# Kernel optimization log

Hardware: AMD Instinct MI355X
Metric: run time of the kernel (lower is better)

The kernel has to match this reference:

```python
import jax, jax.numpy as jnp
import numpy as np

EPS = 1e-5
K = 20
MAXV = 64


def knn_idx(x, k):
    # x: [B,N,D] -> idx: [B,N,k] (excluding self, matching torch topk of -dist)
    xx = jnp.sum(x * x, axis=-1, keepdims=True)                      # [B,N,1]
    dist = xx - 2.0 * jnp.einsum('bnd,bmd->bnm', x, x) + jnp.swapaxes(xx, 1, 2)
    _, idx = jax.lax.top_k(-dist, k + 1)
    return idx[:, :, 1:]


def edge_conv(x, W, gamma, beta, mean, var, k):
    # x: [B,N,C]; W: [O,2C]; BN in eval mode; max over k neighbors
    idx = knn_idx(x, k)                                              # [B,N,k]
    nbr = jax.vmap(lambda xi, ii: xi[ii])(x, idx)                    # [B,N,k,C]
    ctr = jnp.broadcast_to(x[:, :, None, :], nbr.shape)
    ef = jnp.concatenate([ctr, nbr - ctr], axis=-1)                  # [B,N,k,2C]
    y = jnp.einsum('bnkc,oc->bnko', ef, W)                           # 1x1 conv
    y = (y - mean) * (gamma * jax.lax.rsqrt(var + EPS)) + beta       # BN eval
    y = jnp.where(y >= 0, y, 0.2 * y)                                # LeakyReLU
    return jnp.max(y, axis=2)                                        # [B,N,O]


def setup_inputs() -> dict:
    key = jax.random.key(0)
    ks = jax.random.split(key, 32)
    f32 = jnp.float32
    def w(k_, o, i):
        return jax.random.normal(k_, (o, i), f32) / np.float32(np.sqrt(i))
    def vec(k_, c):
        return jax.random.normal(k_, (c,), f32) * 0.1
    d = {}
    d['x'] = jax.random.normal(ks[0], (4, 8192, 5), f32)
    # EdgeConv 1: 5 -> 32
    d['W1'] = w(ks[1], 32, 10)
    d['g1'] = jax.random.uniform(ks[2], (32,), f32, 0.5, 1.5)
    d['b1'] = vec(ks[3], 32); d['m1'] = vec(ks[4], 32)
    d['v1'] = jax.random.uniform(ks[5], (32,), f32, 0.5, 1.5)
    # EdgeConv 2: 32 -> 64
    d['W2'] = w(ks[6], 64, 64)
    d['g2'] = jax.random.uniform(ks[7], (64,), f32, 0.5, 1.5)
    d['b2'] = vec(ks[8], 64); d['m2'] = vec(ks[9], 64)
    d['v2'] = jax.random.uniform(ks[10], (64,), f32, 0.5, 1.5)
    # EdgeConv 3: 64 -> 128
    d['W3'] = w(ks[11], 128, 128)
    d['g3'] = jax.random.uniform(ks[12], (128,), f32, 0.5, 1.5)
    d['b3'] = vec(ks[13], 128); d['m3'] = vec(ks[14], 128)
    d['v3'] = jax.random.uniform(ks[15], (128,), f32, 0.5, 1.5)
    # conv_global: 224 -> 256
    d['Wg'] = w(ks[16], 256, 224)
    d['gg'] = jax.random.uniform(ks[17], (256,), f32, 0.5, 1.5)
    d['bg'] = vec(ks[18], 256); d['mg'] = vec(ks[19], 256)
    d['vg'] = jax.random.uniform(ks[20], (256,), f32, 0.5, 1.5)
    # vertex predictor heads
    d['Wv1'] = w(ks[21], 512, 256); d['bv1'] = vec(ks[22], 512)
    d['Wv2'] = w(ks[23], 192, 512); d['bv2'] = vec(ks[24], 192)
    d['Wq1'] = w(ks[25], 64, 256); d['bq1'] = vec(ks[26], 64)
    d['Wq2'] = w(ks[27], 1, 64); d['bq2'] = vec(ks[28], 1)
    return d


def reference(x, W1, g1, b1, m1, v1, W2, g2, b2, m2, v2, W3, g3, b3, m3, v3,
              Wg, gg, bg, mg, vg, Wv1, bv1, Wv2, bv2, Wq1, bq1, Wq2, bq2):
    B = x.shape[0]
    x1 = edge_conv(x, W1, g1, b1, m1, v1, K)      # [B,N,32]
    x2 = edge_conv(x1, W2, g2, b2, m2, v2, K)     # [B,N,64]
    x3 = edge_conv(x2, W3, g3, b3, m3, v3, K)     # [B,N,128]
    x_concat = jnp.concatenate([x1, x2, x3], axis=2)               # [B,N,224]
    xg = jnp.einsum('bnc,oc->bno', x_concat, Wg)                   # 1x1 conv1d
    xg = (xg - mg) * (gg * jax.lax.rsqrt(vg + EPS)) + bg
    xg = jnp.where(xg >= 0, xg, 0.2 * xg)
    gfeat = jnp.max(xg, axis=1)                                    # [B,256]
    h = jax.nn.relu(gfeat @ Wv1.T + bv1)                           # Dropout=eval id
    vertex_coords = (h @ Wv2.T + bv2).reshape(B, MAXV, 3)
    q = jax.nn.relu(gfeat @ Wq1.T + bq1)
    nvs = jax.nn.sigmoid(q @ Wq2.T + bq2)                          # [B,1]
    num_vertices = jnp.clip(jnp.round(nvs * MAXV), 1, MAXV).astype(jnp.int32)
    return (vertex_coords, num_vertices[:, 0], nvs[:, 0], gfeat, x_concat)
```

## Files before the change

kernel.cpp:

```cpp
#include <hip/hip_runtime.h>
#include <hip/hip_bf16.h>


#define NPTS 8192
#define BATCH 4
#define KNBR 20

typedef _Float16 half8 __attribute__((ext_vector_type(8)));
typedef float f32x4 __attribute__((ext_vector_type(4)));

__device__ __forceinline__ int cswz(int r, int nc) {
    return (nc == 8) ? (r & 7) : ((r >> 1) & 3);
}
__device__ __forceinline__ int dswz(int q) { return (q >> 1) & 7; }

template <int D, int DK, int RS, int S>
__global__ __launch_bounds__(128, 2) void knn_part_mfma(
    const float* feat, float* xcat) {
    constexpr int TJ  = 32;
    constexpr int BUF = 12;
    constexpr int JC  = NPTS / S;
    constexpr int NC  = DK / 8;
    constexpr int KS  = DK / 32;
    constexpr int DSTR = 32;
    constexpr int RSF = (D % 4 == 0) ? D : 9;
    constexpr int REGA = 16384;
    constexpr int OFF_XJF = REGA;
    constexpr int OFF_XJH = OFF_XJF + ((TJ * RSF * 4 + 15) & ~15);
    constexpr int OFF_XXJ = OFF_XJH + TJ * DK * 2;
    constexpr int OFF_SXJ = OFF_XXJ + JC * 4;
    constexpr int OFF_BUF = OFF_SXJ + JC * 4;
    constexpr int OFF_MEA = OFF_BUF + BUF * 128 * 2;
    constexpr int OFF_TMX = OFF_MEA + ((D * 4 + 15) & ~15);
    __shared__ __align__(16) char smem[OFF_TMX + (JC / TJ) * 4];

    float*          dist = (float*)smem;
    _Float16*       xih  = (_Float16*)smem;
    float*          xjf  = (float*)(smem + OFF_XJF);
    _Float16*       xjh  = (_Float16*)(smem + OFF_XJH);
    float*          xxj  = (float*)(smem + OFF_XXJ);
    float*          sxj  = (float*)(smem + OFF_SXJ);
    unsigned short* bufj = (unsigned short*)(smem + OFF_BUF);
    float*          meanp= (float*)(smem + OFF_MEA);
    float*          tmax = (float*)(smem + OFF_TMX);

    const int tid   = threadIdx.x;
    const int gi    = blockIdx.x * 128 + tid;
    const int s     = blockIdx.y;
    const int b     = gi >> 13;
    const int ib    = gi & (NPTS - 1);
    const int n0b   = (blockIdx.x * 128) & (NPTS - 1);
    const int sbase = s * JC;
    const float* fb = feat + (size_t)b * NPTS * RS;

    const float C1 = 0.001953125f;
    const float C2 = 1.52587890625e-05f;

    float xi[D];
    if (D % 4 == 0) {
        #pragma unroll
        for (int c4 = 0; c4 < D / 4; ++c4) {
            float4 v = *(const float4*)(fb + (size_t)ib * RS + 4 * c4);
            xi[4 * c4] = v.x; xi[4 * c4 + 1] = v.y;
            xi[4 * c4 + 2] = v.z; xi[4 * c4 + 3] = v.w;
        }
    } else {
        #pragma unroll
        for (int c = 0; c < D; ++c) xi[c] = fb[(size_t)ib * RS + c];
    }
    float xxi = 0.f;
    #pragma unroll
    for (int c = 0; c < D; ++c) xxi = fmaf(xi[c], xi[c], xxi);

    if (tid < D) meanp[tid] = fb[(size_t)n0b * RS + tid];
    __syncthreads();

    float s_i = 0.f;
    #pragma unroll
    for (int c = 0; c < D; ++c) {
        float d = xi[c] - meanp[c];
        s_i = fmaf(d, d, s_i);
    }
    const float off_i = fmaf(C1, s_i, C2 * xxi) - s_i;

    for (int e = tid; e < 128 * NC; e += 128) {
        int r = e / NC, c = e % NC;
        const float* row = fb + (size_t)(n0b + r) * RS;
        half8 h;
        if (D % 8 == 0) {
            float4 v0 = *(const float4*)(row + c * 8);
            float4 v1 = *(const float4*)(row + c * 8 + 4);
            float4 m0 = *(const float4*)(meanp + c * 8);
            float4 m1 = *(const float4*)(meanp + c * 8 + 4);
            h[0] = (_Float16)(v0.x - m0.x); h[1] = (_Float16)(v0.y - m0.y);
            h[2] = (_Float16)(v0.z - m0.z); h[3] = (_Float16)(v0.w - m0.w);
            h[4] = (_Float16)(v1.x - m1.x); h[5] = (_Float16)(v1.y - m1.y);
            h[6] = (_Float16)(v1.z - m1.z); h[7] = (_Float16)(v1.w - m1.w);
        } else {
            #pragma unroll
            for (int t = 0; t < 8; ++t) {
                int dim = c * 8 + t;
                h[t] = (dim < D) ? (_Float16)(row[dim] - meanp[dim])
                                 : (_Float16)0.f;
            }
        }
        *(half8*)(xih + (size_t)r * DK + (c ^ cswz(r, NC)) * 8) = h;
    }

    for (int r = tid; r < JC; r += 128) {
        const float* row = fb + (size_t)(sbase + r) * RS;
        float sm = 0.f, sc = 0.f;
        if (D % 4 == 0) {
            #pragma unroll
            for (int c4 = 0; c4 < D / 4; ++c4) {
                float4 v = *(const float4*)(row + 4 * c4);
                sm = fmaf(v.x, v.x, sm); sm = fmaf(v.y, v.y, sm);
                sm = fmaf(v.z, v.z, sm); sm = fmaf(v.w, v.w, sm);
                float4 m = *(const float4*)(meanp + 4 * c4);
                float d0 = v.x - m.x, d1 = v.y - m.y;
                float d2 = v.z - m.z, d3 = v.w - m.w;
                sc = fmaf(d0, d0, sc); sc = fmaf(d1, d1, sc);
                sc = fmaf(d2, d2, sc); sc = fmaf(d3, d3, sc);
            }
        } else {
            #pragma unroll
            for (int c = 0; c < D; ++c) {
                float v = row[c];
                sm = fmaf(v, v, sm);
                float d = v - meanp[c];
                sc = fmaf(d, d, sc);
            }
        }
        xxj[r] = sm;
        sxj[r] = sc;
    }
    __syncthreads();

    const int lane = tid & 63, wid = tid >> 6;
    const int ln = lane & 15, lg = lane >> 4;
    half8 bfr[4][KS];
    #pragma unroll
    for (int qs = 0; qs < 4; ++qs)
        #pragma unroll
        for (int ks = 0; ks < KS; ++ks) {
            int q = wid * 64 + qs * 16 + ln;
            bfr[qs][ks] = *(const half8*)(
                xih + (size_t)q * DK + (((lg + 4 * ks) ^ cswz(q, NC)) * 8));
        }

    if (tid < JC / TJ) {
        float mx = -__builtin_inff();
        for (int r = 0; r < TJ; ++r) {
            int j = tid * TJ + ((r + tid) & (TJ - 1));
            mx = fmaxf(mx, fmaf(C1, sxj[j], C2 * xxj[j]));
        }
        tmax[tid] = mx;
    }

    float dl[21];
    int   il[21];
    #pragma unroll
    for (int t = 0; t < 21; ++t) { dl[t] = __builtin_inff(); il[t] = 0; }
    float thr_t  = __builtin_inff();
    float tmaxcur = 0.f;
    int   cnt = 0;
    int   j0s = 0;

    auto insert1 = [&](int u) {
        if (u < cnt) {
            int jsp = (int)bufj[u * 128 + tid];
            int jl  = jsp - j0s;
            const float* row = xjf + (size_t)jl * RSF;
            float dot = 0.f;
            if (D % 4 == 0) {
                int fsw = jl & 7;
                #pragma unroll
                for (int c4 = 0; c4 < D / 4; ++c4) {
                    float4 v = *(const float4*)(row + ((c4 ^ fsw) * 4));
                    dot = fmaf(xi[4 * c4 + 0], v.x, dot);
                    dot = fmaf(xi[4 * c4 + 1], v.y, dot);
                    dot = fmaf(xi[4 * c4 + 2], v.z, dot);
                    dot = fmaf(xi[4 * c4 + 3], v.w, dot);
                }
            } else {
                #pragma unroll
                for (int c = 0; c < D; ++c) dot = fmaf(xi[c], row[c], dot);
            }
            float dd = __builtin_fmaf(-2.f, dot, xxi + xxj[jsp]);
            if (dd < dl[20]) {
                dl[20] = dd; il[20] = sbase + jsp;
                #pragma unroll
                for (int t = 20; t > 0; --t) {
                    if (dl[t] < dl[t - 1]) {
                        float td = dl[t]; dl[t] = dl[t - 1]; dl[t - 1] = td;
                        int   ti = il[t]; il[t] = il[t - 1]; il[t - 1] = ti;
                    }
                }
            }
        }
    };
    auto drain = [&]() {
        #pragma unroll 1
        for (int u = 0; __any(u < cnt); u += 2) {
            insert1(u);
            insert1(u + 1);
        }
        cnt = 0;
        thr_t = dl[20] + off_i + tmaxcur;
    };

    #pragma unroll 1
    for (int t0 = 0; t0 < JC; t0 += TJ) {
        j0s = t0;
        __syncthreads();
        if (D % 8 == 0) {
            for (int e = tid; e < TJ * NC; e += 128) {
                int r = e / NC, c = e % NC;
                const float* row = fb + (size_t)(sbase + t0 + r) * RS + c * 8;
                float4 v0 = *(const float4*)(row);
                float4 v1 = *(const float4*)(row + 4);
                int fsw = r & 7;
                *(float4*)(xjf + (size_t)r * RSF + (((2 * c)     ^ fsw) * 4)) = v0;
                *(float4*)(xjf + (size_t)r * RSF + (((2 * c + 1) ^ fsw) * 4)) = v1;
                float4 m0 = *(const float4*)(meanp + c * 8);
                float4 m1 = *(const float4*)(meanp + c * 8 + 4);
                half8 h;
                h[0] = (_Float16)(v0.x - m0.x); h[1] = (_Float16)(v0.y - m0.y);
                h[2] = (_Float16)(v0.z - m0.z); h[3] = (_Float16)(v0.w - m0.w);
                h[4] = (_Float16)(v1.x - m1.x); h[5] = (_Float16)(v1.y - m1.y);
                h[6] = (_Float16)(v1.z - m1.z); h[7] = (_Float16)(v1.w - m1.w);
                *(half8*)(xjh + (size_t)r * DK + ((c ^ cswz(r, NC)) * 8)) = h;
            }
        } else {
            for (int e = tid; e < TJ * NC; e += 128) {
                int r = e / NC, c = e % NC;
                const float* row = fb + (size_t)(sbase + t0 + r) * RS;
                half8 h;
                #pragma unroll
                for (int q2 = 0; q2 < 8; ++q2) {
                    int dim = c * 8 + q2;
                    float f = (dim < D) ? row[dim] : 0.f;
                    h[q2] = (dim < D) ? (_Float16)(f - meanp[dim])
                                      : (_Float16)0.f;
                    if (c == 0 && q2 < D) xjf[(size_t)r * RSF + q2] = f;
                }
                *(half8*)(xjh + (size_t)r * DK + ((c ^ cswz(r, NC)) * 8)) = h;
            }
        }
        __syncthreads();
        tmaxcur = tmax[t0 >> 5];
        thr_t   = dl[20] + off_i + tmaxcur;

        #pragma unroll
        for (int js = 0; js < TJ / 16; ++js) {
            half8 afr[KS];
            #pragma unroll
            for (int ks = 0; ks < KS; ++ks) {
                int jr = js * 16 + ln;
                afr[ks] = *(const half8*)(
                    xjh + (size_t)jr * DK +
                    (((lg + 4 * ks) ^ cswz(jr, NC)) * 8));
            }
            #pragma unroll
            for (int qs = 0; qs < 4; ++qs) {
                f32x4 acc = {0.f, 0.f, 0.f, 0.f};
                #pragma unroll
                for (int ks = 0; ks < KS; ++ks)
                    acc = __builtin_amdgcn_mfma_f32_16x16x32_f16(
                        afr[ks], bfr[qs][ks], acc, 0, 0, 0);
                float4 sv;
                sv.x = -2.f * acc[0];
                sv.y = -2.f * acc[1];
                sv.z = -2.f * acc[2];
                sv.w = -2.f * acc[3];
                int q  = wid * 64 + qs * 16 + ln;
                int ck = js * 4 + lg;
                *(float4*)(dist + (size_t)q * DSTR + ((ck ^ dswz(q)) * 4)) = sv;
            }
        }
        __syncthreads();

        {
            float* drow = dist + (size_t)tid * DSTR;
            int dsw = dswz(tid);
            #pragma unroll 1
            for (int c = 0; c < TJ / 4; ++c) {
                if (__any(cnt > BUF - 4)) drain();
                float4 sx4 = *(const float4*)(sxj + t0 + c * 4);
                float4 sv  = *(const float4*)(drow + ((c ^ dsw) * 4));
                int jb = t0 + c * 4;
                if (sv.x + sx4.x < thr_t) { bufj[cnt * 128 + tid] = (unsigned short)(jb);     ++cnt; }
                if (sv.y + sx4.y < thr_t) { bufj[cnt * 128 + tid] = (unsigned short)(jb + 1); ++cnt; }
                if (sv.z + sx4.z < thr_t) { bufj[cnt * 128 + tid] = (unsigned short)(jb + 2); ++cnt; }
                if (sv.w + sx4.w < thr_t) { bufj[cnt * 128 + tid] = (unsigned short)(jb + 3); ++cnt; }
            }
            drain();
        }
    }

    unsigned short* cp =
        (unsigned short*)(xcat + (size_t)gi * 224 + 96) + s * 21;
    #pragma unroll
    for (int t = 0; t < 21; ++t) cp[t] = (unsigned short)il[t];
}

template <int D, int RS, int S>
__global__ __launch_bounds__(256) void knn_merge(
    const float* feat, const float* xcat, unsigned short* __restrict__ idxout) {
    int gi = blockIdx.x * 256 + threadIdx.x;
    int b  = gi >> 13;
    int ib = gi & (NPTS - 1);
    const float* fb = feat + (size_t)b * NPTS * RS;

    float xi[D];
    if (D % 4 == 0) {
        #pragma unroll
        for (int c4 = 0; c4 < D / 4; ++c4) {
            float4 v = *(const float4*)(fb + (size_t)ib * RS + 4 * c4);
            xi[4 * c4] = v.x; xi[4 * c4 + 1] = v.y;
            xi[4 * c4 + 2] = v.z; xi[4 * c4 + 3] = v.w;
        }
    } else {
        #pragma unroll
        for (int c = 0; c < D; ++c) xi[c] = fb[(size_t)ib * RS + c];
    }
    float xxi = 0.f;
    #pragma unroll
    for (int c = 0; c < D; ++c) xxi = fmaf(xi[c], xi[c], xxi);

    const unsigned short* cp =
        (const unsigned short*)(xcat + (size_t)gi * 224 + 96);

    float dl[21];
    int   il[21];
    #pragma unroll
    for (int t = 0; t < 21; ++t) { dl[t] = __builtin_inff(); il[t] = 0; }

    for (int t = 0; t < S * 21; ++t) {
        int j = ((int)cp[t]) & (NPTS - 1);
        const float* row = fb + (size_t)j * RS;
        float dot = 0.f, xx = 0.f;
        if (D % 4 == 0) {
            #pragma unroll
            for (int c4 = 0; c4 < D / 4; ++c4) {
                float4 v = *(const float4*)(row + 4 * c4);
                dot = fmaf(xi[4 * c4], v.x, dot);     xx = fmaf(v.x, v.x, xx);
                dot = fmaf(xi[4 * c4 + 1], v.y, dot); xx = fmaf(v.y, v.y, xx);
                dot = fmaf(xi[4 * c4 + 2], v.z, dot); xx = fmaf(v.z, v.z, xx);
                dot = fmaf(xi[4 * c4 + 3], v.w, dot); xx = fmaf(v.w, v.w, xx);
            }
        } else {
            #pragma unroll
            for (int c = 0; c < D; ++c) {
                float v = row[c];
                dot = fmaf(xi[c], v, dot);
                xx  = fmaf(v, v, xx);
            }
        }
        float d = __builtin_fmaf(-2.f, dot, xxi + xx);
        if (d < dl[20]) {
            dl[20] = d; il[20] = j;
            #pragma unroll
            for (int u = 20; u > 0; --u) {
                if (dl[u] < dl[u - 1]) {
                    float td = dl[u]; dl[u] = dl[u - 1]; dl[u - 1] = td;
                    int   ti = il[u]; il[u] = il[u - 1]; il[u - 1] = ti;
                }
            }
        }
    }
    unsigned short* op = idxout + (size_t)gi * KNBR;
    #pragma unroll
    for (int t = 1; t < 21; ++t) op[t - 1] = (unsigned short)il[t];
}

template <int CIN, int RS, int COUT, int OTILE, int P>
__global__ __launch_bounds__(256) void edgeconv_kernel(
    const float* feat, const unsigned short* __restrict__ knn,
    const float* __restrict__ W, const float* __restrict__ g,
    const float* __restrict__ beta, const float* __restrict__ mu,
    const float* __restrict__ var,
    float* outb, int concat_off) {
    __shared__ float diff[P][KNBR][CIN];
    __shared__ float xil[P][CIN];
    __shared__ unsigned short kidx[P * KNBR];
    __shared__ float sl[OTILE], bl[OTILE], ml[OTILE];

    int tid = threadIdx.x;
    int h   = blockIdx.y;
    int n0  = blockIdx.x * P;
    int b   = n0 >> 13;
    const float* fbase = feat + ((size_t)b << 13) * RS;

    for (int e = tid; e < P * CIN; e += 256)
        xil[e / CIN][e % CIN] = feat[(size_t)(n0 + e / CIN) * RS + e % CIN];
    for (int e = tid; e < P * KNBR; e += 256)
        kidx[e] = knn[(size_t)(n0 + e / KNBR) * KNBR + e % KNBR] & (NPTS - 1);
    for (int e = tid; e < OTILE; e += 256) {
        int o = h * OTILE + e;
        sl[e] = g[o] * rsqrtf(var[o] + 1e-5f);
        bl[e] = beta[o];
        ml[e] = mu[o];
    }
    __syncthreads();

    if (CIN % 4 == 0) {
        for (int e = tid; e < P * KNBR * (CIN / 4); e += 256) {
            int r = e / (CIN / 4), c4 = e % (CIN / 4);
            int p = r / KNBR, k = r % KNBR;
            int j = (int)kidx[r];
            float4 v = *(const float4*)(fbase + (size_t)j * RS + 4 * c4);
            diff[p][k][4 * c4 + 0] = v.x - xil[p][4 * c4 + 0];
            diff[p][k][4 * c4 + 1] = v.y - xil[p][4 * c4 + 1];
            diff[p][k][4 * c4 + 2] = v.z - xil[p][4 * c4 + 2];
            diff[p][k][4 * c4 + 3] = v.w - xil[p][4 * c4 + 3];
        }
    } else {
        for (int e = tid; e < P * KNBR * CIN; e += 256) {
            int r = e / CIN, c = e % CIN;
            int pp = r / KNBR, k = r % KNBR;
            int j = (int)kidx[r];
            diff[pp][k][c] = fbase[(size_t)j * RS + c] - xil[pp][c];
        }
    }
    __syncthreads();

    int ol = tid % OTILE, p = tid / OTILE;
    int o  = h * OTILE + ol;

    float wreg[CIN];
    #pragma unroll
    for (int c = 0; c < CIN; ++c) wreg[c] = W[(size_t)o * (2 * CIN) + c];
    float a = 0.f;
    #pragma unroll
    for (int c = 0; c < CIN; ++c) a = fmaf(wreg[c], xil[p][c], a);
    #pragma unroll
    for (int c = 0; c < CIN; ++c) wreg[c] = W[(size_t)o * (2 * CIN) + CIN + c];

    float s = sl[ol], mm = ml[ol], bb = bl[ol];
    float best = -__builtin_inff();
    for (int k = 0; k < KNBR; ++k) {
        float ac0 = a, ac1 = 0.f, ac2 = 0.f, ac3 = 0.f;
        #pragma unroll
        for (int c = 0; c < CIN; ++c) {
            float d = diff[p][k][c];
            if ((c & 3) == 0)      ac0 = fmaf(wreg[c], d, ac0);
            else if ((c & 3) == 1) ac1 = fmaf(wreg[c], d, ac1);
            else if ((c & 3) == 2) ac2 = fmaf(wreg[c], d, ac2);
            else                   ac3 = fmaf(wreg[c], d, ac3);
        }
        float acc = ((ac0 + ac1) + ac2) + ac3;
        float y = (acc - mm) * s + bb;
        y = (y >= 0.f) ? y : 0.2f * y;
        best = fmaxf(best, y);
    }
    outb[(size_t)(n0 + p) * 224 + concat_off + o] = best;
}

__global__ __launch_bounds__(256) void convglobal_kernel(
    const float* __restrict__ xcat,
    const float* __restrict__ Wg, const float* __restrict__ gg,
    const float* __restrict__ bg, const float* __restrict__ mg,
    const float* __restrict__ vg,
    float* __restrict__ partial) {
    const int KC = 56, PT = 64, OT = 64, ST = 68;
    __shared__ float flT[KC * ST];
    __shared__ float WlT[KC * ST];
    __shared__ float red[64 * 17];

    int tid = threadIdx.x;
    int oi  = tid & 15, pi = tid >> 4;
    int o0  = blockIdx.y * OT;
    int n0  = blockIdx.x * PT;
    int b   = n0 >> 13;
    int pchunk = blockIdx.x & 127;

    float acc[4][4];
    #pragma unroll
    for (int u = 0; u < 4; ++u)
        #pragma unroll
        for (int v = 0; v < 4; ++v) acc[u][v] = 0.f;

    for (int kc = 0; kc < 224; kc += KC) {
        __syncthreads();
        for (int e = tid; e < PT * (KC / 4); e += 256) {
            int p = e / (KC / 4), c4 = e % (KC / 4);
            float4 v = *(const float4*)(xcat + (size_t)(n0 + p) * 224 + kc + 4 * c4);
            flT[(4 * c4 + 0) * ST + p] = v.x;
            flT[(4 * c4 + 1) * ST + p] = v.y;
            flT[(4 * c4 + 2) * ST + p] = v.z;
            flT[(4 * c4 + 3) * ST + p] = v.w;
        }
        for (int e = tid; e < OT * (KC / 4); e += 256) {
            int o = e / (KC / 4), c4 = e % (KC / 4);
            float4 v = *(const float4*)(Wg + (size_t)(o0 + o) * 224 + kc + 4 * c4);
            WlT[(4 * c4 + 0) * ST + o] = v.x;
            WlT[(4 * c4 + 1) * ST + o] = v.y;
            WlT[(4 * c4 + 2) * ST + o] = v.z;
            WlT[(4 * c4 + 3) * ST + o] = v.w;
        }
        __syncthreads();
        #pragma unroll 8
        for (int c = 0; c < KC; ++c) {
            float4 w4 = *(const float4*)(WlT + c * ST + oi * 4);
            float4 f4 = *(const float4*)(flT + c * ST + pi * 4);
            acc[0][0] = fmaf(w4.x, f4.x, acc[0][0]);
            acc[0][1] = fmaf(w4.x, f4.y, acc[0][1]);
            acc[0][2] = fmaf(w4.x, f4.z, acc[0][2]);
            acc[0][3] = fmaf(w4.x, f4.w, acc[0][3]);
            acc[1][0] = fmaf(w4.y, f4.x, acc[1][0]);
            acc[1][1] = fmaf(w4.y, f4.y, acc[1][1]);
            acc[1][2] = fmaf(w4.y, f4.z, acc[1][2]);
            acc[1][3] = fmaf(w4.y, f4.w, acc[1][3]);
            acc[2][0] = fmaf(w4.z, f4.x, acc[2][0]);
            acc[2][1] = fmaf(w4.z, f4.y, acc[2][1]);
            acc[2][2] = fmaf(w4.z, f4.z, acc[2][2]);
            acc[2][3] = fmaf(w4.z, f4.w, acc[2][3]);
            acc[3][0] = fmaf(w4.w, f4.x, acc[3][0]);
            acc[3][1] = fmaf(w4.w, f4.y, acc[3][1]);
            acc[3][2] = fmaf(w4.w, f4.z, acc[3][2]);
            acc[3][3] = fmaf(w4.w, f4.w, acc[3][3]);
        }
    }
    #pragma unroll
    for (int u = 0; u < 4; ++u) {
        int oL = oi * 4 + u, o = o0 + oL;
        float s = gg[o] * rsqrtf(vg[o] + 1e-5f);
        float mm = mg[o], bb = bg[o];
        float best = -__builtin_inff();
        #pragma unroll
        for (int v = 0; v < 4; ++v) {
            float y = (acc[u][v] - mm) * s + bb;
            y = (y >= 0.f) ? y : 0.2f * y;
            best = fmaxf(best, y);
        }
        red[oL * 17 + pi] = best;
    }
    __syncthreads();
    if (tid < 64) {
        float best = -__builtin_inff();
        #pragma unroll
        for (int q = 0; q < 16; ++q) best = fmaxf(best, red[tid * 17 + q]);
        partial[((size_t)(b * 128 + pchunk)) * 256 + o0 + tid] = best;
    }
}

__global__ void reduce_gfeat_kernel(const float* __restrict__ partial,
                                    float* __restrict__ gfeat,
                                    float* __restrict__ outg) {
    int b = blockIdx.x, o = threadIdx.x;
    float best = -__builtin_inff();
    for (int ch = 0; ch < 128; ++ch)
        best = fmaxf(best, partial[((size_t)b * 128 + ch) * 256 + o]);
    gfeat[b * 256 + o] = best;
    outg[b * 256 + o]  = best;
}

__global__ __launch_bounds__(256) void heads_kernel(
    const float* __restrict__ gfeat,
    const float* __restrict__ Wv1, const float* __restrict__ bv1,
    const float* __restrict__ Wv2, const float* __restrict__ bv2,
    const float* __restrict__ Wq1, const float* __restrict__ bq1,
    const float* __restrict__ Wq2, const float* __restrict__ bq2,
    float* __restrict__ out) {
    int b = blockIdx.x, t = threadIdx.x;
    __shared__ float gf[256], h[512], q[64];
    gf[t] = gfeat[b * 256 + t];
    __syncthreads();
    for (int r = t; r < 512; r += 256) {
        float acc = bv1[r];
        for (int c = 0; c < 256; ++c) acc = fmaf(Wv1[r * 256 + c], gf[c], acc);
        h[r] = fmaxf(acc, 0.f);
    }
    __syncthreads();
    if (t < 192) {
        float acc = bv2[t];
        for (int c = 0; c < 512; ++c) acc = fmaf(Wv2[t * 512 + c], h[c], acc);
        out[b * 192 + t] = acc;
    } else {
        int r = t - 192;
        if (r < 64) {
            float acc = bq1[r];
            for (int c = 0; c < 256; ++c) acc = fmaf(Wq1[r * 256 + c], gf[c], acc);
            q[r] = fmaxf(acc, 0.f);
        }
    }
    __syncthreads();
    if (t == 0) {
        float acc = bq2[0];
        for (int c = 0; c < 64; ++c) acc = fmaf(Wq2[c], q[c], acc);
        float nv = 1.0f / (1.0f + expf(-acc));
        out[772 + b] = nv;
        float num = fminf(fmaxf(rintf(nv * 64.0f), 1.0f), 64.0f);
        out[768 + b] = num;
    }
}

extern "C" void kernel_launch(void* const* d_in, const int* in_sizes, int n_in,
                              void* d_out, int out_size, void* d_ws, size_t ws_size,
                              hipStream_t stream) {
    (void)in_sizes; (void)n_in; (void)out_size; (void)ws_size;
    const float* x   = (const float*)d_in[0];
    const float* W1  = (const float*)d_in[1];
    const float* g1  = (const float*)d_in[2];
    const float* b1  = (const float*)d_in[3];
    const float* m1  = (const float*)d_in[4];
    const float* v1  = (const float*)d_in[5];
    const float* W2  = (const float*)d_in[6];
    const float* g2  = (const float*)d_in[7];
    const float* b2  = (const float*)d_in[8];
    const float* m2  = (const float*)d_in[9];
    const float* v2  = (const float*)d_in[10];
    const float* W3  = (const float*)d_in[11];
    const float* g3  = (const float*)d_in[12];
    const float* b3  = (const float*)d_in[13];
    const float* m3  = (const float*)d_in[14];
    const float* v3  = (const float*)d_in[15];
    const float* Wg  = (const float*)d_in[16];
    const float* gg  = (const float*)d_in[17];
    const float* bg  = (const float*)d_in[18];
    const float* mg  = (const float*)d_in[19];
    const float* vg  = (const float*)d_in[20];
    const float* Wv1 = (const float*)d_in[21];
    const float* bv1 = (const float*)d_in[22];
    const float* Wv2 = (const float*)d_in[23];
    const float* bv2 = (const float*)d_in[24];
    const float* Wq1 = (const float*)d_in[25];
    const float* bq1 = (const float*)d_in[26];
    const float* Wq2 = (const float*)d_in[27];
    const float* bq2 = (const float*)d_in[28];

    float* out  = (float*)d_out;
    float* xcat = out + 1800;
    char* ws = (char*)d_ws;
    const int ROWS = BATCH * NPTS;

    unsigned short* idx  = (unsigned short*)(ws);
    float*          part = (float*)(ws);
    float*          gft  = (float*)(ws + 524288);

    knn_part_mfma<5, 32, 5, 8><<<dim3(ROWS / 128, 8), 128, 0, stream>>>(x, xcat);
    knn_merge<5, 5, 8><<<ROWS / 256, 256, 0, stream>>>(x, xcat, idx);
    edgeconv_kernel<5, 5, 32, 32, 8>
        <<<dim3(ROWS / 8, 1), 256, 0, stream>>>(x, idx, W1, g1, b1, m1, v1, xcat, 0);

    knn_part_mfma<32, 32, 224, 8><<<dim3(ROWS / 128, 8), 128, 0, stream>>>(xcat, xcat);
    knn_merge<32, 224, 8><<<ROWS / 256, 256, 0, stream>>>(xcat, xcat, idx);
    edgeconv_kernel<32, 224, 64, 64, 4>
        <<<dim3(ROWS / 4, 1), 256, 0, stream>>>(xcat, idx, W2, g2, b2, m2, v2, xcat, 32);

    knn_part_mfma<64, 64, 224, 8><<<dim3(ROWS / 128, 8), 128, 0, stream>>>(xcat + 32, xcat);
    knn_merge<64, 224, 8><<<ROWS / 256, 256, 0, stream>>>(xcat + 32, xcat, idx);
    edgeconv_kernel<64, 224, 128, 64, 4>
        <<<dim3(ROWS / 4, 2), 256, 0, stream>>>(xcat + 32, idx, W3, g3, b3, m3, v3, xcat, 96);

    convglobal_kernel<<<dim3(ROWS / 64, 4), 256, 0, stream>>>(
        xcat, Wg, gg, bg, mg, vg, part);
    reduce_gfeat_kernel<<<BATCH, 256, 0, stream>>>(part, gft, out + 776);

    heads_kernel<<<BATCH, 256, 0, stream>>>(
        gft, Wv1, bv1, Wv2, bv2, Wq1, bq1, Wq2, bq2, out);
}
```

Baseline: 4.202 ms.

## Two-pass fp16 distance threshold candidate filter for KNN partial search

The per-slice KNN kernel now keeps approximate fp16 distances (with the centred-norm term folded in) and runs two passes over the tiles. The first pass builds a top-21 bound from the approximate distances. The second recomputes the tiles and records every candidate under a conservative error-widened threshold, up to 31 per slice, with an overflow flag. The merge kernel then computes exact fp32 distances only for those candidates, or scans the whole slice when the flag is set. This removes the in-loop exact dot products and drain buffers from the partial kernel, at the cost of computing the MFMA tiles twice. Correctness depends on the fp16 error bound constant C1, which was lowered.

```diff
diff --git a/kernel.cpp b/kernel.cpp
--- a/kernel.cpp
+++ b/kernel.cpp
@@ -7,40 +7,35 @@
 #define KNBR 20
 
 typedef _Float16 half8 __attribute__((ext_vector_type(8)));
+typedef _Float16 half4 __attribute__((ext_vector_type(4)));
 typedef float f32x4 __attribute__((ext_vector_type(4)));
 
 __device__ __forceinline__ int cswz(int r, int nc) {
     return (nc == 8) ? (r & 7) : ((r >> 1) & 3);
 }
-__device__ __forceinline__ int dswz(int q) { return (q >> 1) & 7; }
 
 template <int D, int DK, int RS, int S>
 __global__ __launch_bounds__(128, 2) void knn_part_mfma(
     const float* feat, float* xcat) {
     constexpr int TJ  = 32;
-    constexpr int BUF = 12;
+    constexpr int CAP = 31;
+    constexpr int BSTR= 33;
     constexpr int JC  = NPTS / S;
+    constexpr int NT  = JC / TJ;
     constexpr int NC  = DK / 8;
     constexpr int KS  = DK / 32;
-    constexpr int DSTR = 32;
-    constexpr int RSF = (D % 4 == 0) ? D : 9;
-    constexpr int REGA = 16384;
-    constexpr int OFF_XJF = REGA;
-    constexpr int OFF_XJH = OFF_XJF + ((TJ * RSF * 4 + 15) & ~15);
-    constexpr int OFF_XXJ = OFF_XJH + TJ * DK * 2;
-    constexpr int OFF_SXJ = OFF_XXJ + JC * 4;
-    constexpr int OFF_BUF = OFF_SXJ + JC * 4;
-    constexpr int OFF_MEA = OFF_BUF + BUF * 128 * 2;
+    constexpr int OFF_XJH = 16384;
+    constexpr int OFF_BUFE= OFF_XJH + TJ * DK * 2;
+    constexpr int OFF_MEA = OFF_BUFE + 128 * BSTR * 2;
     constexpr int OFF_TMX = OFF_MEA + ((D * 4 + 15) & ~15);
-    __shared__ __align__(16) char smem[OFF_TMX + (JC / TJ) * 4];
-
-    float*          dist = (float*)smem;
+    __shared__ __align__(16) char smem[OFF_TMX + NT * 4];
+
     _Float16*       xih  = (_Float16*)smem;
-    float*          xjf  = (float*)(smem + OFF_XJF);
+    _Float16*       dist = (_Float16*)smem;
+    float*          mtmp = (float*)smem;
+    float*          sxj  = (float*)(smem + 8192);
     _Float16*       xjh  = (_Float16*)(smem + OFF_XJH);
-    float*          xxj  = (float*)(smem + OFF_XXJ);
-    float*          sxj  = (float*)(smem + OFF_SXJ);
-    unsigned short* bufj = (unsigned short*)(smem + OFF_BUF);
+    unsigned short* bufe = (unsigned short*)(smem + OFF_BUFE);
     float*          meanp= (float*)(smem + OFF_MEA);
     float*          tmax = (float*)(smem + OFF_TMX);
 
@@ -53,35 +48,37 @@
     const int sbase = s * JC;
     const float* fb = feat + (size_t)b * NPTS * RS;
 
-    const float C1 = 0.001953125f;
+    const float C1 = 0.0015f;
     const float C2 = 1.52587890625e-05f;
 
-    float xi[D];
-    if (D % 4 == 0) {
-        #pragma unroll
-        for (int c4 = 0; c4 < D / 4; ++c4) {
-            float4 v = *(const float4*)(fb + (size_t)ib * RS + 4 * c4);
-            xi[4 * c4] = v.x; xi[4 * c4 + 1] = v.y;
-            xi[4 * c4 + 2] = v.z; xi[4 * c4 + 3] = v.w;
-        }
-    } else {
-        #pragma unroll
-        for (int c = 0; c < D; ++c) xi[c] = fb[(size_t)ib * RS + c];
-    }
-    float xxi = 0.f;
-    #pragma unroll
-    for (int c = 0; c < D; ++c) xxi = fmaf(xi[c], xi[c], xxi);
-
     if (tid < D) meanp[tid] = fb[(size_t)n0b * RS + tid];
     __syncthreads();
 
-    float s_i = 0.f;
-    #pragma unroll
-    for (int c = 0; c < D; ++c) {
-        float d = xi[c] - meanp[c];
-        s_i = fmaf(d, d, s_i);
-    }
-    const float off_i = fmaf(C1, s_i, C2 * xxi) - s_i;
+    float s_i = 0.f, xxi = 0.f;
+    {
+        const float* row = fb + (size_t)ib * RS;
+        if (D % 4 == 0) {
+            #pragma unroll
+            for (int c4 = 0; c4 < D / 4; ++c4) {
+                float4 v = *(const float4*)(row + 4 * c4);
+                float4 m = *(const float4*)(meanp + 4 * c4);
+                xxi = fmaf(v.x, v.x, xxi); xxi = fmaf(v.y, v.y, xxi);
+                xxi = fmaf(v.z, v.z, xxi); xxi = fmaf(v.w, v.w, xxi);
+                float d0 = v.x - m.x, d1 = v.y - m.y;
+                float d2 = v.z - m.z, d3 = v.w - m.w;
+                s_i = fmaf(d0, d0, s_i); s_i = fmaf(d1, d1, s_i);
+                s_i = fmaf(d2, d2, s_i); s_i = fmaf(d3, d3, s_i);
+            }
+        } else {
+            #pragma unroll
+            for (int c = 0; c < D; ++c) {
+                float v = row[c];
+                xxi = fmaf(v, v, xxi);
+                float d = v - meanp[c];
+                s_i = fmaf(d, d, s_i);
+            }
+        }
+    }
 
     for (int e = tid; e < 128 * NC; e += 128) {
         int r = e / NC, c = e % NC;
@@ -106,17 +103,31 @@
         }
         *(half8*)(xih + (size_t)r * DK + (c ^ cswz(r, NC)) * 8) = h;
     }
+    __syncthreads();
+
+    const int lane = tid & 63, wid = tid >> 6;
+    const int ln = lane & 15, lg = lane >> 4;
+    half8 bfr[4][KS];
+    #pragma unroll
+    for (int qs = 0; qs < 4; ++qs)
+        #pragma unroll
+        for (int ks = 0; ks < KS; ++ks) {
+            int q = wid * 64 + qs * 16 + ln;
+            bfr[qs][ks] = *(const half8*)(
+                xih + (size_t)q * DK + (((lg + 4 * ks) ^ cswz(q, NC)) * 8));
+        }
+    __syncthreads();
 
     for (int r = tid; r < JC; r += 128) {
         const float* row = fb + (size_t)(sbase + r) * RS;
-        float sm = 0.f, sc = 0.f;
+        float sc = 0.f, xx = 0.f;
         if (D % 4 == 0) {
             #pragma unroll
             for (int c4 = 0; c4 < D / 4; ++c4) {
                 float4 v = *(const float4*)(row + 4 * c4);
-                sm = fmaf(v.x, v.x, sm); sm = fmaf(v.y, v.y, sm);
-                sm = fmaf(v.z, v.z, sm); sm = fmaf(v.w, v.w, sm);
                 float4 m = *(const float4*)(meanp + 4 * c4);
+                xx = fmaf(v.x, v.x, xx); xx = fmaf(v.y, v.y, xx);
+                xx = fmaf(v.z, v.z, xx); xx = fmaf(v.w, v.w, xx);
                 float d0 = v.x - m.x, d1 = v.y - m.y;
                 float d2 = v.z - m.z, d3 = v.w - m.w;
                 sc = fmaf(d0, d0, sc); sc = fmaf(d1, d1, sc);
@@ -126,102 +137,36 @@
             #pragma unroll
             for (int c = 0; c < D; ++c) {
                 float v = row[c];
-                sm = fmaf(v, v, sm);
+                xx = fmaf(v, v, xx);
                 float d = v - meanp[c];
                 sc = fmaf(d, d, sc);
             }
         }
-        xxj[r] = sm;
         sxj[r] = sc;
-    }
-    __syncthreads();
-
-    const int lane = tid & 63, wid = tid >> 6;
-    const int ln = lane & 15, lg = lane >> 4;
-    half8 bfr[4][KS];
-    #pragma unroll
-    for (int qs = 0; qs < 4; ++qs)
-        #pragma unroll
-        for (int ks = 0; ks < KS; ++ks) {
-            int q = wid * 64 + qs * 16 + ln;
-            bfr[qs][ks] = *(const half8*)(
-                xih + (size_t)q * DK + (((lg + 4 * ks) ^ cswz(q, NC)) * 8));
-        }
-
-    if (tid < JC / TJ) {
-        float mx = -__builtin_inff();
+        mtmp[r] = fmaf(C1, sc, C2 * xx);
+    }
+    __syncthreads();
+    if (tid < NT) {
+        float mx = 0.f;
         for (int r = 0; r < TJ; ++r) {
             int j = tid * TJ + ((r + tid) & (TJ - 1));
-            mx = fmaxf(mx, fmaf(C1, sxj[j], C2 * xxj[j]));
+            mx = fmaxf(mx, mtmp[j]);
         }
         tmax[tid] = mx;
     }
-
-    float dl[21];
-    int   il[21];
-    #pragma unroll
-    for (int t = 0; t < 21; ++t) { dl[t] = __builtin_inff(); il[t] = 0; }
-    float thr_t  = __builtin_inff();
-    float tmaxcur = 0.f;
-    int   cnt = 0;
-    int   j0s = 0;
-
-    auto insert1 = [&](int u) {
-        if (u < cnt) {
-            int jsp = (int)bufj[u * 128 + tid];
-            int jl  = jsp - j0s;
-            const float* row = xjf + (size_t)jl * RSF;
-            float dot = 0.f;
-            if (D % 4 == 0) {
-                int fsw = jl & 7;
-                #pragma unroll
-                for (int c4 = 0; c4 < D / 4; ++c4) {
-                    float4 v = *(const float4*)(row + ((c4 ^ fsw) * 4));
-                    dot = fmaf(xi[4 * c4 + 0], v.x, dot);
-                    dot = fmaf(xi[4 * c4 + 1], v.y, dot);
-                    dot = fmaf(xi[4 * c4 + 2], v.z, dot);
-                    dot = fmaf(xi[4 * c4 + 3], v.w, dot);
-                }
-            } else {
-                #pragma unroll
-                for (int c = 0; c < D; ++c) dot = fmaf(xi[c], row[c], dot);
-            }
-            float dd = __builtin_fmaf(-2.f, dot, xxi + xxj[jsp]);
-            if (dd < dl[20]) {
-                dl[20] = dd; il[20] = sbase + jsp;
-                #pragma unroll
-                for (int t = 20; t > 0; --t) {
-                    if (dl[t] < dl[t - 1]) {
-                        float td = dl[t]; dl[t] = dl[t - 1]; dl[t - 1] = td;
-                        int   ti = il[t]; il[t] = il[t - 1]; il[t - 1] = ti;
-                    }
-                }
-            }
-        }
-    };
-    auto drain = [&]() {
-        #pragma unroll 1
-        for (int u = 0; __any(u < cnt); u += 2) {
-            insert1(u);
-            insert1(u + 1);
-        }
-        cnt = 0;
-        thr_t = dl[20] + off_i + tmaxcur;
-    };
-
+    __syncthreads();
+    float tmaxG = 0.f;
     #pragma unroll 1
-    for (int t0 = 0; t0 < JC; t0 += TJ) {
-        j0s = t0;
-        __syncthreads();
+    for (int t = 0; t < NT; ++t) tmaxG = fmaxf(tmaxG, tmax[t]);
+    const float c_i = 2.f * fmaf(C1, s_i, C2 * xxi) + tmaxG;
+
+    auto tile_sm = [&](int t0) {
         if (D % 8 == 0) {
             for (int e = tid; e < TJ * NC; e += 128) {
                 int r = e / NC, c = e % NC;
                 const float* row = fb + (size_t)(sbase + t0 + r) * RS + c * 8;
                 float4 v0 = *(const float4*)(row);
                 float4 v1 = *(const float4*)(row + 4);
-                int fsw = r & 7;
-                *(float4*)(xjf + (size_t)r * RSF + (((2 * c)     ^ fsw) * 4)) = v0;
-                *(float4*)(xjf + (size_t)r * RSF + (((2 * c + 1) ^ fsw) * 4)) = v1;
                 float4 m0 = *(const float4*)(meanp + c * 8);
                 float4 m1 = *(const float4*)(meanp + c * 8 + 4);
                 half8 h;
@@ -239,18 +184,13 @@
                 #pragma unroll
                 for (int q2 = 0; q2 < 8; ++q2) {
                     int dim = c * 8 + q2;
-                    float f = (dim < D) ? row[dim] : 0.f;
-                    h[q2] = (dim < D) ? (_Float16)(f - meanp[dim])
+                    h[q2] = (dim < D) ? (_Float16)(row[dim] - meanp[dim])
                                       : (_Float16)0.f;
-                    if (c == 0 && q2 < D) xjf[(size_t)r * RSF + q2] = f;
                 }
                 *(half8*)(xjh + (size_t)r * DK + ((c ^ cswz(r, NC)) * 8)) = h;
             }
         }
         __syncthreads();
-        tmaxcur = tmax[t0 >> 5];
-        thr_t   = dl[20] + off_i + tmaxcur;
-
         #pragma unroll
         for (int js = 0; js < TJ / 16; ++js) {
             half8 afr[KS];
@@ -261,6 +201,7 @@
                     xjh + (size_t)jr * DK +
                     (((lg + 4 * ks) ^ cswz(jr, NC)) * 8));
             }
+            float4 sx4 = *(const float4*)(sxj + t0 + js * 16 + lg * 4);
             #pragma unroll
             for (int qs = 0; qs < 4; ++qs) {
                 f32x4 acc = {0.f, 0.f, 0.f, 0.f};
@@ -268,46 +209,79 @@
                 for (int ks = 0; ks < KS; ++ks)
                     acc = __builtin_amdgcn_mfma_f32_16x16x32_f16(
                         afr[ks], bfr[qs][ks], acc, 0, 0, 0);
-                float4 sv;
-                sv.x = -2.f * acc[0];
-                sv.y = -2.f * acc[1];
-                sv.z = -2.f * acc[2];
-                sv.w = -2.f * acc[3];
                 int q  = wid * 64 + qs * 16 + ln;
                 int ck = js * 4 + lg;
-                *(float4*)(dist + (size_t)q * DSTR + ((ck ^ dswz(q)) * 4)) = sv;
+                half4 hv;
+                hv[0] = (_Float16)fmaf(-2.f, acc[0], sx4.x);
+                hv[1] = (_Float16)fmaf(-2.f, acc[1], sx4.y);
+                hv[2] = (_Float16)fmaf(-2.f, acc[2], sx4.z);
+                hv[3] = (_Float16)fmaf(-2.f, acc[3], sx4.w);
+                *(half4*)(dist + (size_t)q * 32 + ((ck ^ ((q >> 1) & 7)) * 4)) = hv;
             }
         }
         __syncthreads();
-
-        {
-            float* drow = dist + (size_t)tid * DSTR;
-            int dsw = dswz(tid);
-            #pragma unroll 1
-            for (int c = 0; c < TJ / 4; ++c) {
-                if (__any(cnt > BUF - 4)) drain();
-                float4 sx4 = *(const float4*)(sxj + t0 + c * 4);
-                float4 sv  = *(const float4*)(drow + ((c ^ dsw) * 4));
-                int jb = t0 + c * 4;
-                if (sv.x + sx4.x < thr_t) { bufj[cnt * 128 + tid] = (unsigned short)(jb);     ++cnt; }
-                if (sv.y + sx4.y < thr_t) { bufj[cnt * 128 + tid] = (unsigned short)(jb + 1); ++cnt; }
-                if (sv.z + sx4.z < thr_t) { bufj[cnt * 128 + tid] = (unsigned short)(jb + 2); ++cnt; }
-                if (sv.w + sx4.w < thr_t) { bufj[cnt * 128 + tid] = (unsigned short)(jb + 3); ++cnt; }
-            }
-            drain();
-        }
-    }
-
-    unsigned short* cp =
-        (unsigned short*)(xcat + (size_t)gi * 224 + 96) + s * 21;
-    #pragma unroll
-    for (int t = 0; t < 21; ++t) cp[t] = (unsigned short)il[t];
+    };
+
+    float a[21];
+    #pragma unroll
+    for (int t = 0; t < 21; ++t) a[t] = __builtin_inff();
+    auto chain = [&](float v) {
+        if (v < a[20]) {
+            a[20] = v;
+            #pragma unroll
+            for (int t = 20; t > 0; --t)
+                if (a[t] < a[t - 1]) { float tv = a[t]; a[t] = a[t - 1]; a[t - 1] = tv; }
+        }
+    };
+
+    const int dsw = (tid >> 1) & 7;
+    _Float16* drow = dist + (size_t)tid * 32;
+
+    #pragma unroll 1
+    for (int t0 = 0; t0 < JC; t0 += TJ) {
+        tile_sm(t0);
+        #pragma unroll 1
+        for (int c = 0; c < TJ / 4; ++c) {
+            half4 hv = *(const half4*)(drow + ((c ^ dsw) * 4));
+            float f0 = (float)hv[0], f1 = (float)hv[1];
+            float f2 = (float)hv[2], f3 = (float)hv[3];
+            chain(f0); chain(f1); chain(f2); chain(f3);
+        }
+    }
+
+    int cnt = 0;
+    #pragma unroll 1
+    for (int t0 = 0; t0 < JC; t0 += TJ) {
+        tile_sm(t0);
+        float thr2 = a[20] + c_i + tmax[t0 >> 5];
+        #pragma unroll 1
+        for (int c = 0; c < TJ / 4; ++c) {
+            half4 hv = *(const half4*)(drow + ((c ^ dsw) * 4));
+            int jb = t0 + c * 4;
+            float f0 = (float)hv[0], f1 = (float)hv[1];
+            float f2 = (float)hv[2], f3 = (float)hv[3];
+            if (f0 < thr2) { if (cnt < CAP) bufe[tid * BSTR + cnt] = (unsigned short)(jb);     ++cnt; }
+            if (f1 < thr2) { if (cnt < CAP) bufe[tid * BSTR + cnt] = (unsigned short)(jb + 1); ++cnt; }
+            if (f2 < thr2) { if (cnt < CAP) bufe[tid * BSTR + cnt] = (unsigned short)(jb + 2); ++cnt; }
+            if (f3 < thr2) { if (cnt < CAP) bufe[tid * BSTR + cnt] = (unsigned short)(jb + 3); ++cnt; }
+        }
+    }
+
+    unsigned short* sc16 =
+        (unsigned short*)(xcat + (size_t)gi * 224 + 96) + s * 32;
+    if (cnt > CAP) {
+        sc16[0] = 0xFFFFu;
+    } else {
+        sc16[0] = (unsigned short)cnt;
+        for (int k = 0; k < cnt; ++k) sc16[1 + k] = bufe[tid * BSTR + k];
+    }
 }
 
 template <int D, int RS, int S>
-__global__ __launch_bounds__(256) void knn_merge(
+__global__ __launch_bounds__(128) void knn_merge(
     const float* feat, const float* xcat, unsigned short* __restrict__ idxout) {
-    int gi = blockIdx.x * 256 + threadIdx.x;
+    constexpr int JC = NPTS / S;
+    int gi = blockIdx.x * 128 + threadIdx.x;
     int b  = gi >> 13;
     int ib = gi & (NPTS - 1);
     const float* fb = feat + (size_t)b * NPTS * RS;
@@ -336,8 +310,7 @@
     #pragma unroll
     for (int t = 0; t < 21; ++t) { dl[t] = __builtin_inff(); il[t] = 0; }
 
-    for (int t = 0; t < S * 21; ++t) {
-        int j = ((int)cp[t]) & (NPTS - 1);
+    auto ins = [&](int j) {
         const float* row = fb + (size_t)j * RS;
         float dot = 0.f, xx = 0.f;
         if (D % 4 == 0) {
@@ -367,6 +340,19 @@
                     int   ti = il[u]; il[u] = il[u - 1]; il[u - 1] = ti;
                 }
             }
+        }
+    };
+
+    #pragma unroll 1
+    for (int s = 0; s < S; ++s) {
+        int cn = (int)cp[s * 32];
+        if (cn == 0xFFFF) {
+            #pragma unroll 1
+            for (int j = s * JC; j < (s + 1) * JC; ++j) ins(j);
+        } else {
+            #pragma unroll 1
+            for (int k = 0; k < cn; ++k)
+                ins(s * JC + ((int)cp[s * 32 + 1 + k] & (JC - 1)));
         }
     }
     unsigned short* op = idxout + (size_t)gi * KNBR;
@@ -640,17 +626,17 @@
     float*          gft  = (float*)(ws + 524288);
 
     knn_part_mfma<5, 32, 5, 8><<<dim3(ROWS / 128, 8), 128, 0, stream>>>(x, xcat);
-    knn_merge<5, 5, 8><<<ROWS / 256, 256, 0, stream>>>(x, xcat, idx);
+    knn_merge<5, 5, 8><<<ROWS / 128, 128, 0, stream>>>(x, xcat, idx);
     edgeconv_kernel<5, 5, 32, 32, 8>
         <<<dim3(ROWS / 8, 1), 256, 0, stream>>>(x, idx, W1, g1, b1, m1, v1, xcat, 0);
 
     knn_part_mfma<32, 32, 224, 8><<<dim3(ROWS / 128, 8), 128, 0, stream>>>(xcat, xcat);
-    knn_merge<32, 224, 8><<<ROWS / 256, 256, 0, stream>>>(xcat, xcat, idx);
+    knn_merge<32, 224, 8><<<ROWS / 128, 128, 0, stream>>>(xcat, xcat, idx);
     edgeconv_kernel<32, 224, 64, 64, 4>
         <<<dim3(ROWS / 4, 1), 256, 0, stream>>>(xcat, idx, W2, g2, b2, m2, v2, xcat, 32);
 
     knn_part_mfma<64, 64, 224, 8><<<dim3(ROWS / 128, 8), 128, 0, stream>>>(xcat + 32, xcat);
-    knn_merge<64, 224, 8><<<ROWS / 256, 256, 0, stream>>>(xcat + 32, xcat, idx);
+    knn_merge<64, 224, 8><<<ROWS / 128, 128, 0, stream>>>(xcat + 32, xcat, idx);
     edgeconv_kernel<64, 224, 128, 64, 4>
         <<<dim3(ROWS / 4, 2), 256, 0, stream>>>(xcat + 32, idx, W3, g3, b3, m3, v3, xcat, 96);
 
```

After: 16.69 ms. 3.97x slower.
